# Optimization experiments

Measured on AMD Instinct MI355X. Metric: run time of the kernel, lower is better.

Reference implementation:

```python
import jax, jax.numpy as jnp
import numpy as np

VX, VY, VZ = 0.2, 0.2, 4.0
PCR = (0.0, -40.0, -3.0, 70.4, 40.0, 1.0)
X_OFF = VX / 2 + PCR[0]
Y_OFF = VY / 2 + PCR[1]
Z_OFF = VZ / 2 + PCR[2]
BN_EPS = 1e-3
N_POINTS = 600000
N_VOXELS = 60000
CANVAS_X, CANVAS_Y = 352, 400  # (70.4-0)/0.2, (40-(-40))/0.2


def setup_inputs() -> dict:
    key = jax.random.key(0)
    ks = jax.random.split(key, 8)
    rng = np.random.default_rng(0)
    # pick N_VOXELS distinct occupied voxels on the BEV canvas
    lin = rng.permutation(CANVAS_X * CANVAS_Y)[:N_VOXELS]
    inv = rng.integers(0, N_VOXELS, size=N_POINTS)
    inv[:N_VOXELS] = np.arange(N_VOXELS)  # guarantee every voxel occupied
    pv = lin[inv]
    coors = np.zeros((N_POINTS, 4), np.int32)  # (batch, z, y, x)
    coors[:, 3] = pv % CANVAS_X
    coors[:, 2] = pv // CANVAS_X
    # point features: xyz inside point cloud range + intensity
    px = jax.random.uniform(ks[0], (N_POINTS,), minval=PCR[0], maxval=PCR[3])
    py = jax.random.uniform(ks[1], (N_POINTS,), minval=PCR[1], maxval=PCR[4])
    pz = jax.random.uniform(ks[2], (N_POINTS,), minval=PCR[2], maxval=PCR[5])
    pi = jax.random.uniform(ks[3], (N_POINTS,))
    features = jnp.stack([px, py, pz, pi], axis=1)
    return {
        'features': features,
        'w0': jax.random.normal(ks[4], (10, 64)) * 0.3,
        'g0': jnp.ones((64,)),
        'b0': jnp.zeros((64,)),
        'w1': jax.random.normal(ks[5], (128, 128)) * 0.08,
        'g1': jnp.ones((128,)),
        'b1': jnp.zeros((128,)),
        'coors': jnp.asarray(coors),
        'unq_inv': jnp.asarray(inv.astype(np.int32)),
        'num_voxels': N_VOXELS,
    }


def _bn_relu(x, g, b):
    # BN1d training-mode forward: biased batch stats, eps=1e-3
    mu = jnp.mean(x, axis=0)
    var = jnp.mean(jnp.square(x - mu), axis=0)
    return jax.nn.relu((x - mu) * jax.lax.rsqrt(var + BN_EPS) * g + b)


def reference(features, w0, g0, b0, w1, g1, b1, coors, unq_inv, num_voxels):
    n = features.shape[0]
    cf = coors.astype(features.dtype)
    # cluster center: scatter-mean of point features per voxel, gathered back
    vsum = jax.ops.segment_sum(features, unq_inv, num_segments=num_voxels)
    cnt = jax.ops.segment_sum(jnp.ones((n, 1), features.dtype), unq_inv,
                              num_segments=num_voxels)
    voxel_mean = vsum / jnp.maximum(cnt, 1.0)
    f_cluster = features[:, :3] - voxel_mean[unq_inv][:, :3]
    # offset to voxel center (coors layout: batch, z, y, x)
    f_center = jnp.stack([
        features[:, 0] - (cf[:, 3] * VX + X_OFF),
        features[:, 1] - (cf[:, 2] * VY + Y_OFF),
        features[:, 2] - (cf[:, 1] * VZ + Z_OFF),
    ], axis=1)
    x = jnp.concatenate([features, f_cluster, f_center], axis=1)  # [N,10]
    # VFE layer 0 + scatter-max pool + gather-concat
    p0 = _bn_relu(x @ w0, g0, b0)                                  # [N,64]
    v0 = jax.ops.segment_max(p0, unq_inv, num_segments=num_voxels)
    x1 = jnp.concatenate([p0, v0[unq_inv]], axis=1)                # [N,128]
    # VFE layer 1 + final scatter-max pool
    p1 = _bn_relu(x1 @ w1, g1, b1)                                 # [N,128]
    voxel_feats = jax.ops.segment_max(p1, unq_inv, num_segments=num_voxels)
    return voxel_feats  # [M,128]
```

## Files before the change

kernel.cpp:

```cpp
#include <hip/hip_runtime.h>
#include <hip/hip_bf16.h>


typedef __attribute__((ext_vector_type(8))) short bf16x8;
typedef __attribute__((ext_vector_type(4))) float f32x4;
typedef __attribute__((ext_vector_type(4))) int i32x4;
typedef unsigned short u16;
typedef unsigned int u32;

#define RSP 72
#define SCB 2048
#define SPW0 10
#define SPW1 10

__device__ __forceinline__ float bf2f(u16 u) { return __uint_as_float(((u32)u) << 16); }
__device__ __forceinline__ u16 f2bfbits(float f) {
  __hip_bfloat16 h = __float2bfloat16(f);
  return __builtin_bit_cast(u16, h);
}
__device__ __forceinline__ float ldf(const void* p, int i, int flag) {
  return flag ? bf2f(((const u16*)p)[i]) : ((const float*)p)[i];
}
__device__ __forceinline__ u32 encf(float f) {
  u32 b = __float_as_uint(f);
  return b ^ ((u32)(((int)b) >> 31) | 0x80000000u);
}
__device__ __forceinline__ float decf(u32 k) {
  u32 b = (k & 0x80000000u) ? (k ^ 0x80000000u) : ~k;
  return __uint_as_float(b);
}
__device__ __forceinline__ u32 bflyu(u32 x) {
  x = max(x, (u32)__shfl_xor((int)x, 16));
  x = max(x, (u32)__shfl_xor((int)x, 32));
  return x;
}
__device__ __forceinline__ float bflyf(float x) {
  x = fmaxf(x, __shfl_xor(x, 16));
  x = fmaxf(x, __shfl_xor(x, 32));
  return x;
}

__device__ __forceinline__ void compute_x(
    int p, const void* __restrict__ feat, const int4* __restrict__ coors4,
    const int* __restrict__ inv, const float* __restrict__ vsum,
    const unsigned* __restrict__ vcnt, int flag, float x[10]) {
  float px, py, pz, pi;
  if (flag) {
    ushort4 f = ((const ushort4*)feat)[p];
    px = bf2f(f.x); py = bf2f(f.y); pz = bf2f(f.z); pi = bf2f(f.w);
  } else {
    float4 f = ((const float4*)feat)[p];
    px = f.x; py = f.y; pz = f.z; pi = f.w;
  }
  int4 c = coors4[p];
  int v = inv[p];
  unsigned cn = vcnt[v];
  float cnt = (float)(cn ? cn : 1u);
  float mx = vsum[3 * v + 0] / cnt;
  float my = vsum[3 * v + 1] / cnt;
  float mz = vsum[3 * v + 2] / cnt;
  x[0] = px; x[1] = py; x[2] = pz; x[3] = pi;
  x[4] = px - mx; x[5] = py - my; x[6] = pz - mz;
  x[7] = px - ((float)c.w * 0.2f + 0.1f);
  x[8] = py - ((float)c.z * 0.2f - 39.9f);
  x[9] = pz - ((float)c.y * 4.0f - 1.0f);
}

__global__ void k_probe(const u32* __restrict__ g0bits, int* __restrict__ flag) {
  if (threadIdx.x == 0 && blockIdx.x == 0)
    flag[0] = (g0bits[0] == 0x3F800000u) ? 0 : 1;
}

__global__ __launch_bounds__(256) void k_pre(
    const void* __restrict__ w0p, const void* __restrict__ w1p,
    const void* __restrict__ g1p,
    u16* __restrict__ w0t, u16* __restrict__ w1t, u32* __restrict__ gsign,
    float4* __restrict__ z4a, long nza4,
    float4* __restrict__ keysws, float4* __restrict__ doutp, long nzk4,
    const int* __restrict__ flagp) {
  const int t = threadIdx.x;
  const int flag = flagp[0];
  if (blockIdx.x == 0) {
    for (int i = t; i < 2048; i += 256) {
      int c = i >> 5, k = i & 31;
      w0t[i] = (k < 10) ? f2bfbits(ldf(w0p, k * 64 + c, flag)) : (u16)0;
    }
    for (int i = t; i < 16384; i += 256) {
      int c = i >> 7, k = i & 127;
      w1t[i] = f2bfbits(ldf(w1p, k * 128 + c, flag));
    }
    if (t < 128) gsign[t] = (ldf(g1p, t, flag) < 0.f) ? 0xFFFFFFFFu : 0u;
  } else {
    float4* keys4 = flag ? keysws : doutp;
    const long total = nza4 + nzk4;
    const long nth = (long)(gridDim.x - 1) * 256;
    const float4 z = {0.f, 0.f, 0.f, 0.f};
    for (long i = (long)(blockIdx.x - 1) * 256 + t; i < total; i += nth) {
      if (i < nza4) z4a[i] = z; else keys4[i - nza4] = z;
    }
  }
}

__global__ __launch_bounds__(256) void k_hist(const int* __restrict__ inv,
                                              unsigned* __restrict__ vcnt, int n) {
  const int stride = gridDim.x * blockDim.x;
  for (int p = blockIdx.x * blockDim.x + threadIdx.x; p < n; p += stride)
    atomicAdd(&vcnt[inv[p]], 1u);
}

__global__ __launch_bounds__(256) void k_scanA(const unsigned* __restrict__ vcnt,
                                               unsigned* __restrict__ bsum, int M) {
  __shared__ unsigned sh[4];
  const int t = threadIdx.x;
  long base = (long)blockIdx.x * SCB;
  unsigned s = 0;
  for (int i = t; i < SCB; i += 256) {
    long idx = base + i;
    s += (idx < M) ? vcnt[idx] : 0u;
  }
  #pragma unroll
  for (int off = 1; off < 64; off <<= 1) s += __shfl_xor(s, off);
  if ((t & 63) == 0) sh[t >> 6] = s;
  __syncthreads();
  if (t == 0) bsum[blockIdx.x] = sh[0] + sh[1] + sh[2] + sh[3];
}

__global__ __launch_bounds__(256) void k_scanB(const unsigned* __restrict__ bsum,
                                               unsigned* __restrict__ boff, int nb) {
  __shared__ unsigned sh[256];
  const int t = threadIdx.x;
  unsigned loc[8];
  unsigned s = 0;
  #pragma unroll
  for (int j = 0; j < 8; ++j) {
    int i = t * 8 + j;
    loc[j] = (i < nb) ? bsum[i] : 0u;
    s += loc[j];
  }
  sh[t] = s; __syncthreads();
  for (int off = 1; off < 256; off <<= 1) {
    unsigned add = (t >= off) ? sh[t - off] : 0u;
    __syncthreads();
    sh[t] += add;
    __syncthreads();
  }
  unsigned excl = sh[t] - s;
  #pragma unroll
  for (int j = 0; j < 8; ++j) {
    int i = t * 8 + j;
    if (i < nb) { boff[i] = excl; excl += loc[j]; }
  }
}

__global__ __launch_bounds__(256) void k_scanC(const unsigned* __restrict__ vcnt,
                                               const unsigned* __restrict__ boff,
                                               unsigned* __restrict__ voff, int M) {
  __shared__ unsigned sh[256];
  const int t = threadIdx.x;
  long base = (long)blockIdx.x * SCB;
  unsigned loc[8];
  unsigned s = 0;
  #pragma unroll
  for (int j = 0; j < 8; ++j) {
    long i = base + t * 8 + j;
    loc[j] = (i < M) ? vcnt[i] : 0u;
    s += loc[j];
  }
  sh[t] = s; __syncthreads();
  for (int off = 1; off < 256; off <<= 1) {
    unsigned add = (t >= off) ? sh[t - off] : 0u;
    __syncthreads();
    sh[t] += add;
    __syncthreads();
  }
  unsigned excl = sh[t] - s + boff[blockIdx.x];
  #pragma unroll
  for (int j = 0; j < 8; ++j) {
    long i = base + t * 8 + j;
    if (i < M) { voff[i] = excl; excl += loc[j]; }
  }
}

__global__ __launch_bounds__(256) void k_fill(
    const int* __restrict__ inv, const unsigned* __restrict__ voff,
    unsigned* __restrict__ wcur, int* __restrict__ plist,
    unsigned* __restrict__ pt2pos, int n) {
  const int stride = gridDim.x * blockDim.x;
  for (int p = blockIdx.x * blockDim.x + threadIdx.x; p < n; p += stride) {
    int v = inv[p];
    unsigned pos = voff[v] + atomicAdd(&wcur[v], 1u);
    plist[pos] = p;
    pt2pos[p] = pos;
  }
}

__global__ __launch_bounds__(256) void k_vsum(
    const void* __restrict__ feat, const int* __restrict__ plist,
    const unsigned* __restrict__ voff, const unsigned* __restrict__ vcnt,
    float* __restrict__ vsum, const int* __restrict__ flagp, int M) {
  const int flag = flagp[0];
  const int v = blockIdx.x * 256 + threadIdx.x;
  if (v >= M) return;
  const unsigned o = voff[v], c = vcnt[v];
  float sx = 0.f, sy = 0.f, sz = 0.f;
  for (unsigned j = 0; j < c; ++j) {
    int pid = plist[o + j];
    if (flag) {
      ushort4 f = ((const ushort4*)feat)[pid];
      sx += bf2f(f.x); sy += bf2f(f.y); sz += bf2f(f.z);
    } else {
      float4 f = ((const float4*)feat)[pid];
      sx += f.x; sy += f.y; sz += f.z;
    }
  }
  vsum[3 * v + 0] = sx;
  vsum[3 * v + 1] = sy;
  vsum[3 * v + 2] = sz;
}

__global__ __launch_bounds__(256) void k_fillx(
    const void* __restrict__ feat, const int4* __restrict__ coors4,
    const int* __restrict__ inv, const float* __restrict__ vsum,
    const unsigned* __restrict__ vcnt, const unsigned* __restrict__ pt2pos,
    u32* __restrict__ xpk, float* __restrict__ stat0acc,
    const int* __restrict__ flagp, int n) {
  const int flag = flagp[0];
  float acc[65];
  #pragma unroll
  for (int j = 0; j < 65; ++j) acc[j] = 0.f;
  const int t = threadIdx.x;
  const int stride = gridDim.x * blockDim.x;
  for (int p = blockIdx.x * blockDim.x + t; p < n; p += stride) {
    float x[10];
    compute_x(p, feat, coors4, inv, vsum, vcnt, flag, x);
    const int v = inv[p];
    int k = 0;
    #pragma unroll
    for (int a = 0; a < 10; ++a) acc[k++] += x[a];
    #pragma unroll
    for (int a = 0; a < 10; ++a) {
      #pragma unroll
      for (int b = a; b < 10; ++b) acc[k++] += x[a] * x[b];
    }
    u32 u[5];
    #pragma unroll
    for (int j = 0; j < 5; ++j)
      u[j] = (u32)f2bfbits(x[2 * j]) | ((u32)f2bfbits(x[2 * j + 1]) << 16);
    const unsigned pos = pt2pos[p];
    uint4* dst = (uint4*)(xpk + (long)pos * 8);
    uint4 q0 = {u[0], u[1], u[2], u[3]};
    uint4 q1 = {u[4], (u32)v, 0u, 0u};
    dst[0] = q0;
    dst[1] = q1;
  }
  __shared__ float red[65];
  if (t < 65) red[t] = 0.f;
  __syncthreads();
  const int lane = t & 63;
  #pragma unroll
  for (int j = 0; j < 65; ++j) {
    float s = acc[j];
    #pragma unroll
    for (int off = 1; off < 64; off <<= 1) s += __shfl_xor(s, off);
    if (lane == 0) atomicAdd(&red[j], s);
  }
  __syncthreads();
  if (t < 65) atomicAdd(&stat0acc[t], red[t]);
}

__global__ void k_bn0fin(const float* __restrict__ stat0acc,
                         const void* __restrict__ w0p,
                         const void* __restrict__ g0p,
                         const void* __restrict__ b0p,
                         float* __restrict__ a0, float* __restrict__ c0,
                         const int* __restrict__ flagp, int n) {
  const int flag = flagp[0];
  __shared__ float tot[65];
  const int t = threadIdx.x;
  if (t < 65) tot[t] = stat0acc[t];
  __syncthreads();
  if (t < 64) {
    const float invN = 1.0f / (float)n;
    float w[10];
    #pragma unroll
    for (int i = 0; i < 10; ++i) w[i] = ldf(w0p, i * 64 + t, flag);
    float mu = 0.f;
    #pragma unroll
    for (int i = 0; i < 10; ++i) mu += tot[i] * w[i];
    mu *= invN;
    float e2 = 0.f;
    int k = 10;
    #pragma unroll
    for (int a = 0; a < 10; ++a) {
      #pragma unroll
      for (int b = a; b < 10; ++b) {
        float term = tot[k++] * invN * w[a] * w[b];
        e2 += (a == b) ? term : 2.0f * term;
      }
    }
    float var = fmaxf(e2 - mu * mu, 0.f);
    float rs = 1.0f / sqrtf(var + 1e-3f);
    float aa = ldf(g0p, t, flag) * rs;
    a0[t] = aa;
    c0[t] = ldf(b0p, t, flag) - mu * aa;
  }
}

__device__ __forceinline__ bf16x8 l0frag(const u32* __restrict__ xpk,
                                         long grow, long n, int kg) {
  i32x4 ai = {0, 0, 0, 0};
  if (grow < n) {
    const u32* rp = xpk + grow * 8;
    if (kg == 0) {
      uint4 q = *(const uint4*)rp;
      ai[0] = (int)q.x; ai[1] = (int)q.y; ai[2] = (int)q.z; ai[3] = (int)q.w;
    } else if (kg == 1) {
      ai[0] = (int)rp[4];
    }
  }
  return __builtin_bit_cast(bf16x8, ai);
}

__global__ __launch_bounds__(256) void k_l0vox(
    const u32* __restrict__ xpk, const u16* __restrict__ w0t,
    const float* __restrict__ a0, const float* __restrict__ c0,
    float* __restrict__ v0, long n, long nseg, int M) {
  __shared__ int vxs[64];
  __shared__ float pval[2][64];
  __shared__ int pvox[2];
  const int t = threadIdx.x, lane = t & 63, w = t >> 6;
  const int cl = lane & 15, kg = lane >> 4;
  const bf16x8 bw = *(const bf16x8*)(w0t + (16 * w + cl) * 32 + 8 * kg);
  const float al = a0[16 * w + cl], be = c0[16 * w + cl];
  const f32x4 fz = {0.f, 0.f, 0.f, 0.f};
  int curv = -2; float cm = 0.f;
  bool first = true; int fvox = -2; float fcm = 0.f;
  int lastid = -2;
  const long segbase = (long)blockIdx.x * SPW0;
  for (int s = 0; s < SPW0; ++s) {
    const long seg = segbase + s;
    if (seg >= nseg) break;
    const long jb = seg * 64;
    if (t < 64) vxs[t] = (jb + t < n) ? (int)xpk[(jb + t) * 8 + 5] : M;
    __syncthreads();
    for (int mt = 0; mt < 4; ++mt) {
      const long grow = jb + 16 * mt + cl;
      bf16x8 av = l0frag(xpk, grow, n, kg);
      f32x4 a = __builtin_amdgcn_mfma_f32_16x16x32_bf16(av, bw, fz, 0, 0, 0);
      float y[4];
      #pragma unroll
      for (int i2 = 0; i2 < 4; ++i2)
        y[i2] = fmaxf(fmaf(a[i2], al, be), 0.f);
      const int rb = 16 * mt;
      const int rid = vxs[rb + cl];
      const int prid = (cl == 0) ? lastid : vxs[rb + cl - 1];
      const u32 starts = (u32)(__ballot(rid != prid) & 0xFFFFull) | 0x10000u;
      int r = 0;
      while (r < 16) {
        const u32 above = starts & (0xFFFFFFFFu << (r + 1));
        const int e = __ffs(above) - 2;
        const int vrun = __shfl(rid, r);
        float pm = 0.f;
        #pragma unroll
        for (int i2 = 0; i2 < 4; ++i2) {
          const int row = 4 * kg + i2;
          pm = (row >= r && row <= e) ? fmaxf(pm, y[i2]) : pm;
        }
        pm = bflyf(pm);
        if (vrun == curv) cm = fmaxf(cm, pm);
        else {
          if (curv >= 0 && curv < M) {
            if (first) { fvox = curv; fcm = cm; first = false; }
            else if (kg == 0) v0[(long)curv * 64 + 16 * w + cl] = cm;
          }
          curv = vrun; cm = pm;
        }
        r = e + 1;
      }
      lastid = vxs[rb + 15];
    }
    __syncthreads();
  }
  if (t == 0) { pvox[0] = fvox; pvox[1] = curv; }
  if (kg == 0) { pval[0][16 * w + cl] = fcm; pval[1][16 * w + cl] = cm; }
  __syncthreads();
  if (t < 64) {
    int vox = -2; float val = 0.f; bool afirst = true;
    for (int e2 = 0; e2 < 2; ++e2) {
      int ev = pvox[e2];
      if (ev < 0 || ev >= M) continue;
      float evv = pval[e2][t];
      if (ev == vox) val = fmaxf(val, evv);
      else {
        if (vox >= 0) {
          if (afirst) { atomicMax((int*)&v0[(long)vox * 64 + t], __float_as_int(val)); afirst = false; }
          else v0[(long)vox * 64 + t] = val;
        }
        vox = ev; val = evv;
      }
    }
    if (vox >= 0) atomicMax((int*)&v0[(long)vox * 64 + t], __float_as_int(val));
  }
}

__device__ __forceinline__ bf16x8 pack8(float4 a, float4 b) {
  bf16x8 r;
  r[0] = (short)f2bfbits(a.x); r[1] = (short)f2bfbits(a.y);
  r[2] = (short)f2bfbits(a.z); r[3] = (short)f2bfbits(a.w);
  r[4] = (short)f2bfbits(b.x); r[5] = (short)f2bfbits(b.y);
  r[6] = (short)f2bfbits(b.z); r[7] = (short)f2bfbits(b.w);
  return r;
}

__global__ __launch_bounds__(256) void k_vfe1vox(
    const u32* __restrict__ xpk, const u16* __restrict__ w0t,
    const float* __restrict__ a0, const float* __restrict__ c0,
    const u16* __restrict__ w1t, const u32* __restrict__ gsign,
    const float* __restrict__ v0,
    u32* __restrict__ keysws, u32* __restrict__ doutk,
    float* __restrict__ stat1acc,
    const int* __restrict__ flagp, long n, long nseg, int M) {
  const int flag = flagp[0];
  u32* keys = flag ? keysws : doutk;
  __shared__ u16 stg[64 * RSP];
  __shared__ int vxs[64];
  __shared__ u32 pval[2][128];
  __shared__ int pvox[2];
  const int t = threadIdx.x, lane = t & 63, w = t >> 6;
  const int cl = lane & 15, kg = lane >> 4;
  const int ct0 = 2 * w, ct1 = 2 * w + 1;
  bf16x8 bw[4];
  float al[4], be[4];
  #pragma unroll
  for (int ct = 0; ct < 4; ++ct) {
    bw[ct] = *(const bf16x8*)(w0t + (16 * ct + cl) * 32 + 8 * kg);
    al[ct] = a0[16 * ct + cl];
    be[ct] = c0[16 * ct + cl];
  }
  const u32 gs0 = gsign[16 * ct0 + cl], gs1 = gsign[16 * ct1 + cl];
  const u16* wr0 = w1t + (16 * ct0 + cl) * 128 + 8 * kg;
  const u16* wr1 = w1t + (16 * ct1 + cl) * 128 + 8 * kg;
  float ssum0 = 0.f, ssq0 = 0.f, ssum1 = 0.f, ssq1 = 0.f;
  const f32x4 fz = {0.f, 0.f, 0.f, 0.f};
  int curv = -2; u32 cm0 = 0, cm1 = 0;
  bool first = true; int fvox = -2; u32 fm0 = 0, fm1 = 0;
  int lastid = -2;
  const long segbase = (long)blockIdx.x * SPW1;

  for (int s = 0; s < SPW1; ++s) {
    const long seg = segbase + s;
    if (seg >= nseg) break;
    const long jb = seg * 64;
    if (t < 64) vxs[t] = (jb + t < n) ? (int)xpk[(jb + t) * 8 + 5] : M;
    {
      const long grow = jb + 16 * w + cl;
      bf16x8 av = l0frag(xpk, grow, n, kg);
      #pragma unroll
      for (int ct = 0; ct < 4; ++ct) {
        f32x4 a = __builtin_amdgcn_mfma_f32_16x16x32_bf16(av, bw[ct], fz, 0, 0, 0);
        #pragma unroll
        for (int i2 = 0; i2 < 4; ++i2) {
          const int lr = 16 * w + 4 * kg + i2;
          float y = fmaxf(fmaf(a[i2], al[ct], be[ct]), 0.f);
          if (jb + lr >= n) y = 0.f;
          stg[lr * RSP + 16 * ct + cl] = f2bfbits(y);
        }
      }
    }
    __syncthreads();
    for (int q = 0; q < 4; ++q) {
      const int lr = 16 * q + cl;
      bf16x8 afr0 = *(const bf16x8*)&stg[lr * RSP + 8 * kg];
      bf16x8 afr1 = *(const bf16x8*)&stg[lr * RSP + 32 + 8 * kg];
      const int vv = vxs[lr];
      const float* vr = v0 + (long)vv * 64;
      float4 f0 = *(const float4*)(vr + 8 * kg);
      float4 f1 = *(const float4*)(vr + 8 * kg + 4);
      float4 f2 = *(const float4*)(vr + 32 + 8 * kg);
      float4 f3 = *(const float4*)(vr + 32 + 8 * kg + 4);
      bf16x8 afr2 = pack8(f0, f1);
      bf16x8 afr3 = pack8(f2, f3);
      f32x4 acc0 = fz, acc1 = fz;
      {
        bf16x8 b0 = *(const bf16x8*)(wr0);
        bf16x8 b1 = *(const bf16x8*)(wr0 + 32);
        bf16x8 b2 = *(const bf16x8*)(wr0 + 64);
        bf16x8 b3 = *(const bf16x8*)(wr0 + 96);
        acc0 = __builtin_amdgcn_mfma_f32_16x16x32_bf16(afr0, b0, acc0, 0, 0, 0);
        acc0 = __builtin_amdgcn_mfma_f32_16x16x32_bf16(afr1, b1, acc0, 0, 0, 0);
        acc0 = __builtin_amdgcn_mfma_f32_16x16x32_bf16(afr2, b2, acc0, 0, 0, 0);
        acc0 = __builtin_amdgcn_mfma_f32_16x16x32_bf16(afr3, b3, acc0, 0, 0, 0);
      }
      {
        bf16x8 b0 = *(const bf16x8*)(wr1);
        bf16x8 b1 = *(const bf16x8*)(wr1 + 32);
        bf16x8 b2 = *(const bf16x8*)(wr1 + 64);
        bf16x8 b3 = *(const bf16x8*)(wr1 + 96);
        acc1 = __builtin_amdgcn_mfma_f32_16x16x32_bf16(afr0, b0, acc1, 0, 0, 0);
        acc1 = __builtin_amdgcn_mfma_f32_16x16x32_bf16(afr1, b1, acc1, 0, 0, 0);
        acc1 = __builtin_amdgcn_mfma_f32_16x16x32_bf16(afr2, b2, acc1, 0, 0, 0);
        acc1 = __builtin_amdgcn_mfma_f32_16x16x32_bf16(afr3, b3, acc1, 0, 0, 0);
      }
      u32 e0[4], e1[4];
      #pragma unroll
      for (int i2 = 0; i2 < 4; ++i2) {
        float ya = acc0[i2], yb = acc1[i2];
        if (jb + 16 * q + 4 * kg + i2 >= n) { ya = 0.f; yb = 0.f; }
        ssum0 += ya; ssq0 += ya * ya;
        ssum1 += yb; ssq1 += yb * yb;
        e0[i2] = encf(ya) ^ gs0;
        e1[i2] = encf(yb) ^ gs1;
      }
      const int rb = 16 * q;
      const int rid = vxs[rb + cl];
      const int prid = (cl == 0) ? lastid : vxs[rb + cl - 1];
      const u32 starts = (u32)(__ballot(rid != prid) & 0xFFFFull) | 0x10000u;
      int r = 0;
      while (r < 16) {
        const u32 above = starts & (0xFFFFFFFFu << (r + 1));
        const int e = __ffs(above) - 2;
        const int vrun = __shfl(rid, r);
        u32 p0m = 0, p1m = 0;
        #pragma unroll
        for (int i2 = 0; i2 < 4; ++i2) {
          const int row = 4 * kg + i2;
          const bool in = (row >= r) && (row <= e);
          p0m = in ? max(p0m, e0[i2]) : p0m;
          p1m = in ? max(p1m, e1[i2]) : p1m;
        }
        p0m = bflyu(p0m);
        p1m = bflyu(p1m);
        if (vrun == curv) { cm0 = max(cm0, p0m); cm1 = max(cm1, p1m); }
        else {
          if (curv >= 0 && curv < M) {
            if (first) { fvox = curv; fm0 = cm0; fm1 = cm1; first = false; }
            else if (kg == 0) {
              u32* row = keys + (long)curv * 128;
              row[16 * ct0 + cl] = cm0;
              row[16 * ct1 + cl] = cm1;
            }
          }
          curv = vrun; cm0 = p0m; cm1 = p1m;
        }
        r = e + 1;
      }
      lastid = vxs[rb + 15];
    }
    __syncthreads();
  }
  if (t == 0) { pvox[0] = fvox; pvox[1] = curv; }
  if (kg == 0) {
    pval[0][16 * ct0 + cl] = fm0; pval[0][16 * ct1 + cl] = fm1;
    pval[1][16 * ct0 + cl] = cm0; pval[1][16 * ct1 + cl] = cm1;
  }
  __syncthreads();
  if (t < 128) {
    int vox = -2; u32 val = 0; bool afirst = true;
    for (int e2 = 0; e2 < 2; ++e2) {
      int ev = pvox[e2];
      if (ev < 0 || ev >= M) continue;
      u32 evv = pval[e2][t];
      if (ev == vox) val = max(val, evv);
      else {
        if (vox >= 0) {
          if (afirst) { atomicMax(&keys[(long)vox * 128 + t], val); afirst = false; }
          else keys[(long)vox * 128 + t] = val;
        }
        vox = ev; val = evv;
      }
    }
    if (vox >= 0) atomicMax(&keys[(long)vox * 128 + t], val);
  }
  ssum0 += __shfl_xor(ssum0, 16); ssum0 += __shfl_xor(ssum0, 32);
  ssq0 += __shfl_xor(ssq0, 16); ssq0 += __shfl_xor(ssq0, 32);
  ssum1 += __shfl_xor(ssum1, 16); ssum1 += __shfl_xor(ssum1, 32);
  ssq1 += __shfl_xor(ssq1, 16); ssq1 += __shfl_xor(ssq1, 32);
  if (kg == 0) {
    atomicAdd(&stat1acc[16 * ct0 + cl], ssum0);
    atomicAdd(&stat1acc[16 * ct1 + cl], ssum1);
    atomicAdd(&stat1acc[128 + 16 * ct0 + cl], ssq0);
    atomicAdd(&stat1acc[128 + 16 * ct1 + cl], ssq1);
  }
}

__global__ void k_bn1fin(const float* __restrict__ stat1acc,
                         const void* __restrict__ g1p,
                         const void* __restrict__ b1p,
                         float* __restrict__ a1, float* __restrict__ c1,
                         const int* __restrict__ flagp, int n) {
  const int flag = flagp[0];
  const int c = threadIdx.x;
  float s = stat1acc[c];
  float q = stat1acc[128 + c];
  const float invN = 1.0f / (float)n;
  float mu = s * invN;
  float var = fmaxf(q * invN - mu * mu, 0.f);
  float rs = 1.0f / sqrtf(var + 1e-3f);
  float aa = ldf(g1p, c, flag) * rs;
  a1[c] = aa;
  c1[c] = ldf(b1p, c, flag) - mu * aa;
}

__global__ __launch_bounds__(256) void k_fin(
    const u32* __restrict__ keysws, u32* __restrict__ doutk,
    const float* __restrict__ a1, const float* __restrict__ c1,
    const u32* __restrict__ gsign, void* __restrict__ dout,
    const int* __restrict__ flagp, int m32) {
  const int flag = flagp[0];
  const uint4* src = (const uint4*)(flag ? keysws : doutk);
  const int stride = gridDim.x * blockDim.x;
  for (int i = blockIdx.x * blockDim.x + threadIdx.x; i < m32; i += stride) {
    uint4 k = src[i];
    const int cb = (i * 4) & 127;
    float z0 = fmaxf(fmaf(decf(k.x ^ gsign[cb + 0]), a1[cb + 0], c1[cb + 0]), 0.f);
    float z1 = fmaxf(fmaf(decf(k.y ^ gsign[cb + 1]), a1[cb + 1], c1[cb + 1]), 0.f);
    float z2 = fmaxf(fmaf(decf(k.z ^ gsign[cb + 2]), a1[cb + 2], c1[cb + 2]), 0.f);
    float z3 = fmaxf(fmaf(decf(k.w ^ gsign[cb + 3]), a1[cb + 3], c1[cb + 3]), 0.f);
    if (flag) {
      ushort4 o;
      o.x = f2bfbits(z0); o.y = f2bfbits(z1); o.z = f2bfbits(z2); o.w = f2bfbits(z3);
      ((ushort4*)dout)[i] = o;
    } else {
      float4 o = {z0, z1, z2, z3};
      ((float4*)dout)[i] = o;
    }
  }
}

extern "C" void kernel_launch(void* const* d_in, const int* in_sizes, int n_in,
                              void* d_out, int out_size, void* d_ws, size_t ws_size,
                              hipStream_t stream) {
  (void)n_in; (void)ws_size;
  const int n = in_sizes[0] / 4;
  const int M = out_size / 128;
  const long nseg = (n + 63) >> 6;
  const int nb = (M + SCB - 1) / SCB;
  const int nblk0 = (int)((nseg + SPW0 - 1) / SPW0);
  const int nblk1 = (int)((nseg + SPW1 - 1) / SPW1);
  const int nbv = (M + 255) / 256;
  if (n <= 0 || M <= 0) return;

  const void* feat = d_in[0];
  const void* w0p = d_in[1];
  const void* g0p = d_in[2];
  const void* b0p = d_in[3];
  const void* w1p = d_in[4];
  const void* g1p = d_in[5];
  const void* b1p = d_in[6];
  const int4* coors4 = (const int4*)d_in[7];
  const int* inv = (const int*)d_in[8];

  char* wsb = (char*)d_ws;
  long off = 0;
  auto alloc = [&](long bytes) -> void* {
    void* p = wsb + off;
    off = (off + bytes + 255) & ~255L;
    return p;
  };
  int* flagp = (int*)alloc(256);
  float* a0 = (float*)alloc(256);
  float* c0 = (float*)alloc(256);
  float* a1 = (float*)alloc(512);
  float* c1 = (float*)alloc(512);
  u32* gsign = (u32*)alloc(512);
  u16* w0t = (u16*)alloc(2048 * 2);
  u16* w1t = (u16*)alloc(16384 * 2);
  unsigned* bsum = (unsigned*)alloc(2048 * 4);
  unsigned* boff = (unsigned*)alloc(2048 * 4);
  unsigned* voff = (unsigned*)alloc((long)M * 4);
  float* vsum = (float*)alloc((long)M * 3 * 4);
  int* plist = (int*)alloc((long)nseg * 64 * 4);
  unsigned* pt2pos = (unsigned*)alloc((long)n * 4);
  u32* xpk = (u32*)alloc((long)nseg * 64 * 32);
  const long nza = 384L + M + (long)(M + 1) * 64 + M;
  float* zbase = (float*)alloc(((nza + 3) / 4) * 16);
  float* stat0acc = zbase;
  float* stat1acc = zbase + 80;
  unsigned* vcnt = (unsigned*)(zbase + 384);
  float* v0 = (float*)(vcnt + M);
  unsigned* wcur = (unsigned*)(v0 + (long)(M + 1) * 64);
  u32* keysws = (u32*)alloc((long)M * 128 * 4);

  hipLaunchKernelGGL(k_probe, dim3(1), dim3(64), 0, stream, (const u32*)g0p, flagp);
  hipLaunchKernelGGL(k_pre, dim3(2048), dim3(256), 0, stream,
                     w0p, w1p, g1p, w0t, w1t, gsign,
                     (float4*)zbase, (nza + 3) / 4,
                     (float4*)keysws, (float4*)d_out, (long)M * 32, flagp);
  hipLaunchKernelGGL(k_hist, dim3(1024), dim3(256), 0, stream, inv, vcnt, n);
  hipLaunchKernelGGL(k_scanA, dim3(nb), dim3(256), 0, stream, vcnt, bsum, M);
  hipLaunchKernelGGL(k_scanB, dim3(1), dim3(256), 0, stream, bsum, boff, nb);
  hipLaunchKernelGGL(k_scanC, dim3(nb), dim3(256), 0, stream, vcnt, boff, voff, M);
  hipLaunchKernelGGL(k_fill, dim3(1024), dim3(256), 0, stream,
                     inv, voff, wcur, plist, pt2pos, n);
  hipLaunchKernelGGL(k_vsum, dim3(nbv), dim3(256), 0, stream,
                     feat, plist, voff, vcnt, vsum, flagp, M);
  hipLaunchKernelGGL(k_fillx, dim3(1024), dim3(256), 0, stream,
                     feat, coors4, inv, vsum, vcnt, pt2pos, xpk, stat0acc, flagp, n);
  hipLaunchKernelGGL(k_bn0fin, dim3(1), dim3(128), 0, stream,
                     stat0acc, w0p, g0p, b0p, a0, c0, flagp, n);
  hipLaunchKernelGGL(k_l0vox, dim3(nblk0), dim3(256), 0, stream,
                     xpk, w0t, a0, c0, v0, (long)n, nseg, M);
  hipLaunchKernelGGL(k_vfe1vox, dim3(nblk1), dim3(256), 0, stream,
                     xpk, w0t, a0, c0, w1t, gsign, v0,
                     keysws, (u32*)d_out, stat1acc, flagp, (long)n, nseg, M);
  hipLaunchKernelGGL(k_bn1fin, dim3(1), dim3(128), 0, stream,
                     stat1acc, g1p, b1p, a1, c1, flagp, n);
  hipLaunchKernelGGL(k_fin, dim3(1024), dim3(256), 0, stream,
                     keysws, (u32*)d_out, a1, c1, gsign, d_out, flagp, M * 32);
}
```

Measured before the change: 376.8 us.

## Scatter point records into voxel order once and pre-convert v0 to bf16

The fill kernel now writes a voxel-sorted record of each point's features, packed coordinates and voxel id. The voxel-sum and x-building kernels then read that record contiguously instead of gathering features, coords and inv through plist and pt2pos indirection. A new kernel converts the pooled v0 to bf16 once, so the layer-1 kernel loads bf16 fragments directly instead of converting fp32 per row. The SPW0/SPW1 constants are reduced from 10 to 6. Costs are an extra launch, an extra record buffer, and a 10-bit limit on x/y when coordinates are packed.

```diff
diff --git a/kernel.cpp b/kernel.cpp
--- a/kernel.cpp
+++ b/kernel.cpp
@@ -10,8 +10,8 @@
 
 #define RSP 72
 #define SCB 2048
-#define SPW0 10
-#define SPW1 10
+#define SPW0 6
+#define SPW1 6
 
 __device__ __forceinline__ float bf2f(u16 u) { return __uint_as_float(((u32)u) << 16); }
 __device__ __forceinline__ u16 f2bfbits(float f) {
@@ -39,31 +39,13 @@
   x = fmaxf(x, __shfl_xor(x, 32));
   return x;
 }
-
-__device__ __forceinline__ void compute_x(
-    int p, const void* __restrict__ feat, const int4* __restrict__ coors4,
-    const int* __restrict__ inv, const float* __restrict__ vsum,
-    const unsigned* __restrict__ vcnt, int flag, float x[10]) {
-  float px, py, pz, pi;
-  if (flag) {
-    ushort4 f = ((const ushort4*)feat)[p];
-    px = bf2f(f.x); py = bf2f(f.y); pz = bf2f(f.z); pi = bf2f(f.w);
-  } else {
-    float4 f = ((const float4*)feat)[p];
-    px = f.x; py = f.y; pz = f.z; pi = f.w;
-  }
-  int4 c = coors4[p];
-  int v = inv[p];
-  unsigned cn = vcnt[v];
-  float cnt = (float)(cn ? cn : 1u);
-  float mx = vsum[3 * v + 0] / cnt;
-  float my = vsum[3 * v + 1] / cnt;
-  float mz = vsum[3 * v + 2] / cnt;
-  x[0] = px; x[1] = py; x[2] = pz; x[3] = pi;
-  x[4] = px - mx; x[5] = py - my; x[6] = pz - mz;
-  x[7] = px - ((float)c.w * 0.2f + 0.1f);
-  x[8] = py - ((float)c.z * 0.2f - 39.9f);
-  x[9] = pz - ((float)c.y * 4.0f - 1.0f);
+__device__ __forceinline__ bf16x8 pack8(float4 a, float4 b) {
+  bf16x8 r;
+  r[0] = (short)f2bfbits(a.x); r[1] = (short)f2bfbits(a.y);
+  r[2] = (short)f2bfbits(a.z); r[3] = (short)f2bfbits(a.w);
+  r[4] = (short)f2bfbits(b.x); r[5] = (short)f2bfbits(b.y);
+  r[6] = (short)f2bfbits(b.z); r[7] = (short)f2bfbits(b.w);
+  return r;
 }
 
 __global__ void k_probe(const u32* __restrict__ g0bits, int* __restrict__ flag) {
@@ -181,59 +163,76 @@
   }
 }
 
-__global__ __launch_bounds__(256) void k_fill(
+__global__ __launch_bounds__(256) void k_fill2(
+    const void* __restrict__ feat, const int4* __restrict__ coors4,
     const int* __restrict__ inv, const unsigned* __restrict__ voff,
-    unsigned* __restrict__ wcur, int* __restrict__ plist,
-    unsigned* __restrict__ pt2pos, int n) {
+    unsigned* __restrict__ wcur, u32* __restrict__ rec,
+    const int* __restrict__ flagp, int n) {
+  const int flag = flagp[0];
   const int stride = gridDim.x * blockDim.x;
   for (int p = blockIdx.x * blockDim.x + threadIdx.x; p < n; p += stride) {
+    float fx, fy, fz, fi;
+    if (flag) {
+      ushort4 f = ((const ushort4*)feat)[p];
+      fx = bf2f(f.x); fy = bf2f(f.y); fz = bf2f(f.z); fi = bf2f(f.w);
+    } else {
+      float4 f = ((const float4*)feat)[p];
+      fx = f.x; fy = f.y; fz = f.z; fi = f.w;
+    }
+    int4 c = coors4[p];
+    u32 cp = ((u32)(c.y & 0xFFF) << 20) | ((u32)(c.z & 0x3FF) << 10) | (u32)(c.w & 0x3FF);
     int v = inv[p];
     unsigned pos = voff[v] + atomicAdd(&wcur[v], 1u);
-    plist[pos] = p;
-    pt2pos[p] = pos;
-  }
-}
-
-__global__ __launch_bounds__(256) void k_vsum(
-    const void* __restrict__ feat, const int* __restrict__ plist,
-    const unsigned* __restrict__ voff, const unsigned* __restrict__ vcnt,
-    float* __restrict__ vsum, const int* __restrict__ flagp, int M) {
-  const int flag = flagp[0];
+    uint4* dst = (uint4*)(rec + (long)pos * 8);
+    uint4 q0 = {__float_as_uint(fx), __float_as_uint(fy), __float_as_uint(fz), __float_as_uint(fi)};
+    uint4 q1 = {cp, (u32)v, 0u, 0u};
+    dst[0] = q0;
+    dst[1] = q1;
+  }
+}
+
+__global__ __launch_bounds__(256) void k_vsum2(
+    const u32* __restrict__ rec, const unsigned* __restrict__ voff,
+    const unsigned* __restrict__ vcnt, float* __restrict__ vsum, int M) {
   const int v = blockIdx.x * 256 + threadIdx.x;
   if (v >= M) return;
   const unsigned o = voff[v], c = vcnt[v];
   float sx = 0.f, sy = 0.f, sz = 0.f;
   for (unsigned j = 0; j < c; ++j) {
-    int pid = plist[o + j];
-    if (flag) {
-      ushort4 f = ((const ushort4*)feat)[pid];
-      sx += bf2f(f.x); sy += bf2f(f.y); sz += bf2f(f.z);
-    } else {
-      float4 f = ((const float4*)feat)[pid];
-      sx += f.x; sy += f.y; sz += f.z;
-    }
+    const float* rp = (const float*)(rec + (long)(o + j) * 8);
+    sx += rp[0]; sy += rp[1]; sz += rp[2];
   }
   vsum[3 * v + 0] = sx;
   vsum[3 * v + 1] = sy;
   vsum[3 * v + 2] = sz;
 }
 
-__global__ __launch_bounds__(256) void k_fillx(
-    const void* __restrict__ feat, const int4* __restrict__ coors4,
-    const int* __restrict__ inv, const float* __restrict__ vsum,
-    const unsigned* __restrict__ vcnt, const unsigned* __restrict__ pt2pos,
-    u32* __restrict__ xpk, float* __restrict__ stat0acc,
-    const int* __restrict__ flagp, int n) {
-  const int flag = flagp[0];
+__global__ __launch_bounds__(256) void k_fillx2(
+    const u32* __restrict__ rec, const float* __restrict__ vsum,
+    const unsigned* __restrict__ vcnt,
+    u32* __restrict__ xpk, float* __restrict__ stat0acc, int n) {
   float acc[65];
   #pragma unroll
   for (int j = 0; j < 65; ++j) acc[j] = 0.f;
   const int t = threadIdx.x;
   const int stride = gridDim.x * blockDim.x;
-  for (int p = blockIdx.x * blockDim.x + t; p < n; p += stride) {
+  for (int pos = blockIdx.x * blockDim.x + t; pos < n; pos += stride) {
+    const u32* rp = rec + (long)pos * 8;
+    uint4 q0 = *(const uint4*)rp;
+    uint4 q1 = *(const uint4*)(rp + 4);
+    float px = __uint_as_float(q0.x), py = __uint_as_float(q0.y);
+    float pz = __uint_as_float(q0.z), pi = __uint_as_float(q0.w);
+    const u32 cp = q1.x;
+    const int v = (int)q1.y;
+    unsigned cn = vcnt[v];
+    float ic = 1.f / (float)(cn ? cn : 1u);
+    float mx = vsum[3 * v + 0] * ic, my = vsum[3 * v + 1] * ic, mz = vsum[3 * v + 2] * ic;
     float x[10];
-    compute_x(p, feat, coors4, inv, vsum, vcnt, flag, x);
-    const int v = inv[p];
+    x[0] = px; x[1] = py; x[2] = pz; x[3] = pi;
+    x[4] = px - mx; x[5] = py - my; x[6] = pz - mz;
+    x[7] = px - ((float)(cp & 0x3FFu) * 0.2f + 0.1f);
+    x[8] = py - ((float)((cp >> 10) & 0x3FFu) * 0.2f - 39.9f);
+    x[9] = pz - ((float)((cp >> 20) & 0xFFFu) * 4.0f - 1.0f);
     int k = 0;
     #pragma unroll
     for (int a = 0; a < 10; ++a) acc[k++] += x[a];
@@ -246,12 +245,11 @@
     #pragma unroll
     for (int j = 0; j < 5; ++j)
       u[j] = (u32)f2bfbits(x[2 * j]) | ((u32)f2bfbits(x[2 * j + 1]) << 16);
-    const unsigned pos = pt2pos[p];
     uint4* dst = (uint4*)(xpk + (long)pos * 8);
-    uint4 q0 = {u[0], u[1], u[2], u[3]};
-    uint4 q1 = {u[4], (u32)v, 0u, 0u};
-    dst[0] = q0;
-    dst[1] = q1;
+    uint4 o0 = {u[0], u[1], u[2], u[3]};
+    uint4 o1 = {u[4], (u32)v, 0u, 0u};
+    dst[0] = o0;
+    dst[1] = o1;
   }
   __shared__ float red[65];
   if (t < 65) red[t] = 0.f;
@@ -403,20 +401,21 @@
   }
 }
 
-__device__ __forceinline__ bf16x8 pack8(float4 a, float4 b) {
-  bf16x8 r;
-  r[0] = (short)f2bfbits(a.x); r[1] = (short)f2bfbits(a.y);
-  r[2] = (short)f2bfbits(a.z); r[3] = (short)f2bfbits(a.w);
-  r[4] = (short)f2bfbits(b.x); r[5] = (short)f2bfbits(b.y);
-  r[6] = (short)f2bfbits(b.z); r[7] = (short)f2bfbits(b.w);
-  return r;
+__global__ __launch_bounds__(256) void k_v0cvt(const float4* __restrict__ v0,
+                                               bf16x8* __restrict__ v0b, long n8) {
+  const long stride = (long)gridDim.x * blockDim.x;
+  for (long i = (long)blockIdx.x * blockDim.x + threadIdx.x; i < n8; i += stride) {
+    float4 f0 = v0[2 * i];
+    float4 f1 = v0[2 * i + 1];
+    v0b[i] = pack8(f0, f1);
+  }
 }
 
 __global__ __launch_bounds__(256) void k_vfe1vox(
     const u32* __restrict__ xpk, const u16* __restrict__ w0t,
     const float* __restrict__ a0, const float* __restrict__ c0,
     const u16* __restrict__ w1t, const u32* __restrict__ gsign,
-    const float* __restrict__ v0,
+    const u16* __restrict__ v0b,
     u32* __restrict__ keysws, u32* __restrict__ doutk,
     float* __restrict__ stat1acc,
     const int* __restrict__ flagp, long n, long nseg, int M) {
@@ -473,13 +472,9 @@
       bf16x8 afr0 = *(const bf16x8*)&stg[lr * RSP + 8 * kg];
       bf16x8 afr1 = *(const bf16x8*)&stg[lr * RSP + 32 + 8 * kg];
       const int vv = vxs[lr];
-      const float* vr = v0 + (long)vv * 64;
-      float4 f0 = *(const float4*)(vr + 8 * kg);
-      float4 f1 = *(const float4*)(vr + 8 * kg + 4);
-      float4 f2 = *(const float4*)(vr + 32 + 8 * kg);
-      float4 f3 = *(const float4*)(vr + 32 + 8 * kg + 4);
-      bf16x8 afr2 = pack8(f0, f1);
-      bf16x8 afr3 = pack8(f2, f3);
+      const u16* vb = v0b + (long)vv * 64;
+      bf16x8 afr2 = *(const bf16x8*)(vb + 8 * kg);
+      bf16x8 afr3 = *(const bf16x8*)(vb + 32 + 8 * kg);
       f32x4 acc0 = fz, acc1 = fz;
       {
         bf16x8 b0 = *(const bf16x8*)(wr0);
@@ -669,9 +664,9 @@
   unsigned* boff = (unsigned*)alloc(2048 * 4);
   unsigned* voff = (unsigned*)alloc((long)M * 4);
   float* vsum = (float*)alloc((long)M * 3 * 4);
-  int* plist = (int*)alloc((long)nseg * 64 * 4);
-  unsigned* pt2pos = (unsigned*)alloc((long)n * 4);
+  u32* rec = (u32*)alloc((long)nseg * 64 * 32);
   u32* xpk = (u32*)alloc((long)nseg * 64 * 32);
+  u16* v0b = (u16*)alloc((long)(M + 1) * 64 * 2);
   const long nza = 384L + M + (long)(M + 1) * 64 + M;
   float* zbase = (float*)alloc(((nza + 3) / 4) * 16);
   float* stat0acc = zbase;
@@ -690,18 +685,20 @@
   hipLaunchKernelGGL(k_scanA, dim3(nb), dim3(256), 0, stream, vcnt, bsum, M);
   hipLaunchKernelGGL(k_scanB, dim3(1), dim3(256), 0, stream, bsum, boff, nb);
   hipLaunchKernelGGL(k_scanC, dim3(nb), dim3(256), 0, stream, vcnt, boff, voff, M);
-  hipLaunchKernelGGL(k_fill, dim3(1024), dim3(256), 0, stream,
-                     inv, voff, wcur, plist, pt2pos, n);
-  hipLaunchKernelGGL(k_vsum, dim3(nbv), dim3(256), 0, stream,
-                     feat, plist, voff, vcnt, vsum, flagp, M);
-  hipLaunchKernelGGL(k_fillx, dim3(1024), dim3(256), 0, stream,
-                     feat, coors4, inv, vsum, vcnt, pt2pos, xpk, stat0acc, flagp, n);
+  hipLaunchKernelGGL(k_fill2, dim3(1024), dim3(256), 0, stream,
+                     feat, coors4, inv, voff, wcur, rec, flagp, n);
+  hipLaunchKernelGGL(k_vsum2, dim3(nbv), dim3(256), 0, stream,
+                     rec, voff, vcnt, vsum, M);
+  hipLaunchKernelGGL(k_fillx2, dim3(1024), dim3(256), 0, stream,
+                     rec, vsum, vcnt, xpk, stat0acc, n);
   hipLaunchKernelGGL(k_bn0fin, dim3(1), dim3(128), 0, stream,
                      stat0acc, w0p, g0p, b0p, a0, c0, flagp, n);
   hipLaunchKernelGGL(k_l0vox, dim3(nblk0), dim3(256), 0, stream,
                      xpk, w0t, a0, c0, v0, (long)n, nseg, M);
+  hipLaunchKernelGGL(k_v0cvt, dim3(512), dim3(256), 0, stream,
+                     (const float4*)v0, (bf16x8*)v0b, (long)(M + 1) * 8);
   hipLaunchKernelGGL(k_vfe1vox, dim3(nblk1), dim3(256), 0, stream,
-                     xpk, w0t, a0, c0, w1t, gsign, v0,
+                     xpk, w0t, a0, c0, w1t, gsign, v0b,
                      keysws, (u32*)d_out, stat1acc, flagp, (long)n, nseg, M);
   hipLaunchKernelGGL(k_bn1fin, dim3(1), dim3(128), 0, stream,
                      stat1acc, g1p, b1p, a1, c1, flagp, n);
```

Result: no change. 383.2 us (+1.7%).
